# Kernel tuning notes

Measured on AMD Instinct MI355X. Metric: run time of the kernel, lower is better.

Reference implementation:

```python
import jax, jax.numpy as jnp
import numpy as np

B, S, D, H, KD = 4, 2048, 640, 10, 64


def setup_inputs() -> dict:
    key = jax.random.key(0)
    k0, k1, k2, k3, k4 = jax.random.split(key, 5)
    x = jax.random.normal(k0, (B, S, D), dtype=jnp.float32)
    # per-head projection weights, stacked over heads: [H, D, KD]
    Wq = jax.random.normal(k1, (H, D, KD), dtype=jnp.float32) * 0.05
    Wk = jax.random.normal(k2, (H, D, KD), dtype=jnp.float32) * 0.05
    Wv = jax.random.normal(k3, (H, D, KD), dtype=jnp.float32) * 0.05
    # output projection: [H*KD, D]
    Wo = jax.random.normal(k4, (H * KD, D), dtype=jnp.float32) * 0.05
    return {"x": x, "Wq": Wq, "Wk": Wk, "Wv": Wv, "Wo": Wo}


def reference(x, Wq, Wk, Wv, Wo):
    # Batched equivalent of the per-head Python loop:
    # each head computes q=x@Wq_h, k=x@Wk_h, v=x@Wv_h, softmax(q k^T / sqrt(KD)) @ v
    q = jnp.einsum("bsd,hdk->bhsk", x, Wq)
    k = jnp.einsum("bsd,hdk->bhsk", x, Wk)
    v = jnp.einsum("bsd,hdk->bhsk", x, Wv)
    scale = 1.0 / jnp.sqrt(jnp.asarray(KD, x.dtype))
    scores = jnp.einsum("bhsk,bhtk->bhst", q, k) * scale  # [B,H,S,S]
    attn = jax.nn.softmax(scores, axis=-1)
    z = jnp.einsum("bhst,bhtk->bhsk", attn, v)  # [B,H,S,KD]
    # concat heads along last axis (head 0 first, matching the loop order)
    z = z.transpose(0, 2, 1, 3).reshape(x.shape[0], x.shape[1], H * KD)
    return jnp.einsum("bsf,fd->bsd", z, Wo)
```

## Files before the change

kernel.cpp:

```cpp
#include <hip/hip_runtime.h>
#include <hip/hip_bf16.h>

#define B_  4
#define S_  2048
#define D_  640
#define H_  10
#define KD_ 64

typedef __attribute__((ext_vector_type(8))) short  short8;
typedef __attribute__((ext_vector_type(4))) short  short4v;
typedef __attribute__((ext_vector_type(4))) float  floatx4;
typedef __attribute__((ext_vector_type(2))) unsigned int uint2v;
typedef __attribute__((ext_vector_type(4))) unsigned int uint4v;

static __device__ __forceinline__ short f2bf_fast(float f) {
    unsigned int u = __float_as_uint(f);
    u += 0x7fffu + ((u >> 16) & 1u);
    return (short)(u >> 16);
}
static __device__ __forceinline__ unsigned int pack2bf(float a, float b) {
    union { __hip_bfloat162 h; unsigned int u; } c;
    c.h = __float22bfloat162_rn(float2{a, b});
    return c.u;
}
static __device__ __forceinline__ float bf2f(short v) {
    return __uint_as_float(((unsigned int)(unsigned short)v) << 16);
}

static __device__ __forceinline__ void gload_lds16(const void* gp, void* lp) {
    __builtin_amdgcn_global_load_lds(
        (const __attribute__((address_space(1))) unsigned int*)gp,
        (__attribute__((address_space(3))) unsigned int*)lp, 16, 0, 0);
}

__global__ __launch_bounds__(256) void prep(
        const float* __restrict__ x,
        const float* __restrict__ Wq, const float* __restrict__ Wk,
        const float* __restrict__ Wv, const float* __restrict__ Wo,
        short* __restrict__ xb, short* __restrict__ BigT,
        short* __restrict__ WoT) {
    __shared__ float tile[32][33];
    int bid = blockIdx.x;
    if (bid < 5120) {
        int idx = (bid * 256 + threadIdx.x) * 4;
        float4 v = *(const float4*)(x + idx);
        uint2v o;
        o[0] = pack2bf(v.x, v.y);
        o[1] = pack2bf(v.z, v.w);
        *(uint2v*)(xb + idx) = o;
    } else if (bid < 6320) {
        int flat = bid - 5120;
        int bz = flat / 40, rem = flat % 40;
        int by = rem >> 1, bxx = rem & 1;
        int w = bz / 10, h = bz % 10;
        const float* W = ((w == 0) ? Wq : (w == 1) ? Wk : Wv) + h * 640 * 64;
        short* out = BigT + (w * 640 + h * 64) * 640;
        int c0 = bxx * 32;
        int r0 = by * 32;
        int tx = threadIdx.x & 31, ty = threadIdx.x >> 5;
        #pragma unroll
        for (int k = 0; k < 4; ++k)
            tile[ty + 8 * k][tx] = W[(r0 + ty + 8 * k) * 64 + c0 + tx];
        __syncthreads();
        #pragma unroll
        for (int k = 0; k < 4; ++k)
            out[(c0 + ty + 8 * k) * 640 + r0 + tx] = f2bf_fast(tile[tx][ty + 8 * k]);
    } else {
        int flat = bid - 6320;
        int c0 = (flat % 20) * 32;
        int r0 = (flat / 20) * 32;
        int tx = threadIdx.x & 31, ty = threadIdx.x >> 5;
        #pragma unroll
        for (int k = 0; k < 4; ++k)
            tile[ty + 8 * k][tx] = Wo[(r0 + ty + 8 * k) * 640 + c0 + tx];
        __syncthreads();
        #pragma unroll
        for (int k = 0; k < 4; ++k)
            WoT[(c0 + ty + 8 * k) * 640 + r0 + tx] = f2bf_fast(tile[tx][ty + 8 * k]);
    }
}


__global__ __launch_bounds__(256) void qkv_gemm(
        const short* __restrict__ X, const short* __restrict__ BigT,
        short* __restrict__ qb, short* __restrict__ kb, short* __restrict__ vtb) {
    __shared__ __align__(16) short Ab[2][128][32];
    __shared__ __align__(16) short Bb[2][128][32];

    int wave = threadIdx.x >> 6;
    int lane = threadIdx.x & 63;
    int lq = lane & 15, quad = lane >> 4;
    int wm = (wave & 1) * 64, wn = (wave >> 1) * 64;

    int lin = blockIdx.y * 64 + blockIdx.x;
    int tm = ((lin & 7) * 8 + ((lin >> 3) & 7)) * 128;
    int tn = (lin >> 6) * 128;

    int srow = lane >> 2;
    int schunk = (lane & 3) ^ ((lane >> 3) & 3);
    const short* Asrc0 = X    + (tm + wave * 32 + srow) * 640 + schunk * 8;
    const short* Bsrc0 = BigT + (tn + wave * 32 + srow) * 640 + schunk * 8;
    const short* Asrc1 = Asrc0 + 16 * 640;
    const short* Bsrc1 = Bsrc0 + 16 * 640;

    floatx4 acc[4][4];
    for (int a = 0; a < 4; ++a)
        for (int n = 0; n < 4; ++n)
            acc[a][n] = (floatx4){0.f, 0.f, 0.f, 0.f};

    int rsw = (lq >> 1) & 3;

    gload_lds16(Asrc0, &Ab[0][wave * 32][0]);
    gload_lds16(Asrc1, &Ab[0][wave * 32 + 16][0]);
    gload_lds16(Bsrc0, &Bb[0][wave * 32][0]);
    gload_lds16(Bsrc1, &Bb[0][wave * 32 + 16][0]);

    int p = 0;
    bool isV = (tn >= 1280);

    for (int k0 = 0; k0 < 640; k0 += 32) {
        __syncthreads();
        if (k0 + 32 < 640) {
            int pn = p ^ 1;
            gload_lds16(Asrc0 + k0 + 32, &Ab[pn][wave * 32][0]);
            gload_lds16(Asrc1 + k0 + 32, &Ab[pn][wave * 32 + 16][0]);
            gload_lds16(Bsrc0 + k0 + 32, &Bb[pn][wave * 32][0]);
            gload_lds16(Bsrc1 + k0 + 32, &Bb[pn][wave * 32 + 16][0]);
        }

        short8 af[4], bf[4];
        #pragma unroll
        for (int t = 0; t < 4; ++t) {
            af[t] = *(const short8*)(&Ab[p][wm + t * 16 + lq][(quad ^ rsw) * 8]);
            bf[t] = *(const short8*)(&Bb[p][wn + t * 16 + lq][(quad ^ rsw) * 8]);
        }
        if (!isV) {
            #pragma unroll
            for (int mt = 0; mt < 4; ++mt)
                #pragma unroll
                for (int nt = 0; nt < 4; ++nt)
                    acc[mt][nt] = __builtin_amdgcn_mfma_f32_16x16x32_bf16(
                        bf[nt], af[mt], acc[mt][nt], 0, 0, 0);
        } else {
            #pragma unroll
            for (int mt = 0; mt < 4; ++mt)
                #pragma unroll
                for (int nt = 0; nt < 4; ++nt)
                    acc[mt][nt] = __builtin_amdgcn_mfma_f32_16x16x32_bf16(
                        af[mt], bf[nt], acc[mt][nt], 0, 0, 0);
        }
        p ^= 1;
    }

    if (!isV) {
        const float qscale = 0.18033688011112042f;
        short* dst = (tn < 640) ? qb : kb;
        float scale = (tn < 640) ? qscale : 1.0f;
        #pragma unroll
        for (int nt = 0; nt < 4; ++nt) {
            int rem = (tn + wn + nt * 16) % 640;
            int hh = rem / 64;
            int kd0 = (rem % 64) + quad * 4;
            #pragma unroll
            for (int mt = 0; mt < 4; ++mt) {
                int m = tm + wm + mt * 16 + lq;
                int b = m >> 11, s = m & 2047;
                uint2v w;
                w[0] = pack2bf(acc[mt][nt][0] * scale, acc[mt][nt][1] * scale);
                w[1] = pack2bf(acc[mt][nt][2] * scale, acc[mt][nt][3] * scale);
                *(uint2v*)(dst + (((b * H_ + hh) * S_ + s) * KD_ + kd0)) = w;
            }
        }
    } else {
        #pragma unroll
        for (int nt = 0; nt < 4; ++nt) {
            int rem = (tn + wn + nt * 16) - 1280;
            int hh = rem / 64;
            int kd = (rem % 64) + lq;
            #pragma unroll
            for (int mt = 0; mt < 4; ++mt) {
                int s = tm + wm + mt * 16 + quad * 4;
                int b = s >> 11, s0 = s & 2047;
                uint2v w;
                w[0] = pack2bf(acc[mt][nt][0], acc[mt][nt][1]);
                w[1] = pack2bf(acc[mt][nt][2], acc[mt][nt][3]);
                *(uint2v*)(vtb + (((b * H_ + hh) * KD_ + kd) * (long)S_ + s0)) = w;
            }
        }
    }
}

__global__ __launch_bounds__(256, 3) void attn(
        const short* __restrict__ qb, const short* __restrict__ kbuf,
        const short* __restrict__ vtb, short* __restrict__ zp0,
        short* __restrict__ zp1, float* __restrict__ lsvb) {
    __shared__ __align__(16) short Kbuf[2][64][64];
    __shared__ __align__(16) short Vbuf[2][64][64];

    int wave = threadIdx.x >> 6;
    int lane = threadIdx.x & 63;
    int lq = lane & 15, quad = lane >> 4;

    int bx = blockIdx.x;
    int xcd = bx & 7, slot = bx >> 3;
    int bh = xcd * 5 + (slot >> 5);
    int rest = slot & 31;
    int qt = rest >> 1;
    int half = rest & 1;
    int b = bh / 10, h = bh % 10;
    int q0 = qt * 128;

    const short* qp = qb + (b * H_ + h) * S_ * KD_;
    const short* kp = kbuf + (b * H_ + h) * S_ * KD_ + half * 1024 * KD_;
    const short* vp = vtb + (b * H_ + h) * KD_ * S_ + half * 1024;

    int r8 = lane >> 3;
    int g  = (lane & 7) ^ r8;
    const short* kg0 = kp + (wave * 16 + r8) * 64 + g * 8;
    const short* kg1 = kp + (wave * 16 + 8 + r8) * 64 + g * 8;
    const short* vg0 = vp + (wave * 16 + r8) * (long)S_ + g * 8;
    const short* vg1 = vp + (wave * 16 + 8 + r8) * (long)S_ + g * 8;

    short8 qA0, qA1, qB0, qB1;
    {
        int rowA = q0 + wave * 32 + lq;
        qA0 = *(const short8*)(qp + rowA * 64 + quad * 8);
        qA1 = *(const short8*)(qp + rowA * 64 + 32 + quad * 8);
        qB0 = *(const short8*)(qp + (rowA + 16) * 64 + quad * 8);
        qB1 = *(const short8*)(qp + (rowA + 16) * 64 + 32 + quad * 8);
    }

    short8 ones;
    #pragma unroll
    for (int i = 0; i < 8; ++i) ones[i] = (short)0x3F80;

    floatx4 OA[4], OB[4];
    for (int n = 0; n < 4; ++n) {
        OA[n] = (floatx4){0.f, 0.f, 0.f, 0.f};
        OB[n] = (floatx4){0.f, 0.f, 0.f, 0.f};
    }
    floatx4 lsvA = (floatx4){0.f, 0.f, 0.f, 0.f};
    floatx4 lsvB = (floatx4){0.f, 0.f, 0.f, 0.f};

    gload_lds16(kg0, &Kbuf[0][wave * 16][0]);
    gload_lds16(kg1, &Kbuf[0][wave * 16 + 8][0]);
    gload_lds16(vg0, &Vbuf[0][wave * 16][0]);
    gload_lds16(vg1, &Vbuf[0][wave * 16 + 8][0]);

    int p = 0;
    int sw = lq & 7;

    for (int t0 = 0; t0 < 1024; t0 += 64) {
        __syncthreads();

        if (t0 + 64 < 1024) {
            int pn = p ^ 1;
            gload_lds16(kg0 + (t0 + 64) * 64, &Kbuf[pn][wave * 16][0]);
            gload_lds16(kg1 + (t0 + 64) * 64, &Kbuf[pn][wave * 16 + 8][0]);
            gload_lds16(vg0 + (t0 + 64),      &Vbuf[pn][wave * 16][0]);
            gload_lds16(vg1 + (t0 + 64),      &Vbuf[pn][wave * 16 + 8][0]);
        }

        const short* Kb = &Kbuf[p][0][0];
        const short* Vb = &Vbuf[p][0][0];

        floatx4 sTA[4], sTB[4];
        __builtin_amdgcn_s_setprio(1);
        #pragma unroll
        for (int kblk = 0; kblk < 4; ++kblk) {
            const short* krow = Kb + (kblk * 16 + lq) * 64;
            short8 bk0 = *(const short8*)(krow + (quad ^ sw) * 8);
            short8 bk1 = *(const short8*)(krow + ((quad + 4) ^ sw) * 8);
            floatx4 zA = (floatx4){0.f, 0.f, 0.f, 0.f};
            zA = __builtin_amdgcn_mfma_f32_16x16x32_bf16(bk0, qA0, zA, 0, 0, 0);
            sTA[kblk] = __builtin_amdgcn_mfma_f32_16x16x32_bf16(bk1, qA1, zA, 0, 0, 0);
            floatx4 zB = (floatx4){0.f, 0.f, 0.f, 0.f};
            zB = __builtin_amdgcn_mfma_f32_16x16x32_bf16(bk0, qB0, zB, 0, 0, 0);
            sTB[kblk] = __builtin_amdgcn_mfma_f32_16x16x32_bf16(bk1, qB1, zB, 0, 0, 0);
        }
        __builtin_amdgcn_s_setprio(0);

        #pragma unroll
        for (int ts = 0; ts < 2; ++ts) {
            int ka = ts * 2, kc = ts * 2 + 1;
            unsigned int a00 = pack2bf(__builtin_amdgcn_exp2f(sTA[ka][0]),
                                       __builtin_amdgcn_exp2f(sTA[ka][1]));
            unsigned int a01 = pack2bf(__builtin_amdgcn_exp2f(sTA[ka][2]),
                                       __builtin_amdgcn_exp2f(sTA[ka][3]));
            unsigned int a10 = pack2bf(__builtin_amdgcn_exp2f(sTA[kc][0]),
                                       __builtin_amdgcn_exp2f(sTA[kc][1]));
            unsigned int a11 = pack2bf(__builtin_amdgcn_exp2f(sTA[kc][2]),
                                       __builtin_amdgcn_exp2f(sTA[kc][3]));
            uint2v sa0 = __builtin_amdgcn_permlane32_swap(a00, a10, false, false);
            uint2v sa1 = __builtin_amdgcn_permlane32_swap(a01, a11, false, false);
            uint2v wa02 = __builtin_amdgcn_permlane16_swap(sa0[0], sa0[1], false, false);
            uint2v wa13 = __builtin_amdgcn_permlane16_swap(sa1[0], sa1[1], false, false);
            union { unsigned int u[4]; short8 s8; } pfa;
            pfa.u[0] = wa02[0];
            pfa.u[1] = wa13[0];
            pfa.u[2] = wa02[1];
            pfa.u[3] = wa13[1];
            short8 pfA = pfa.s8;
            unsigned int b00 = pack2bf(__builtin_amdgcn_exp2f(sTB[ka][0]),
                                       __builtin_amdgcn_exp2f(sTB[ka][1]));
            unsigned int b01 = pack2bf(__builtin_amdgcn_exp2f(sTB[ka][2]),
                                       __builtin_amdgcn_exp2f(sTB[ka][3]));
            unsigned int b10 = pack2bf(__builtin_amdgcn_exp2f(sTB[kc][0]),
                                       __builtin_amdgcn_exp2f(sTB[kc][1]));
            unsigned int b11 = pack2bf(__builtin_amdgcn_exp2f(sTB[kc][2]),
                                       __builtin_amdgcn_exp2f(sTB[kc][3]));
            uint2v sb0 = __builtin_amdgcn_permlane32_swap(b00, b10, false, false);
            uint2v sb1 = __builtin_amdgcn_permlane32_swap(b01, b11, false, false);
            uint2v wb02 = __builtin_amdgcn_permlane16_swap(sb0[0], sb0[1], false, false);
            uint2v wb13 = __builtin_amdgcn_permlane16_swap(sb1[0], sb1[1], false, false);
            union { unsigned int u[4]; short8 s8; } pfb;
            pfb.u[0] = wb02[0];
            pfb.u[1] = wb13[0];
            pfb.u[2] = wb02[1];
            pfb.u[3] = wb13[1];
            short8 pfB = pfb.s8;

            __builtin_amdgcn_s_setprio(1);
            lsvA = __builtin_amdgcn_mfma_f32_16x16x32_bf16(ones, pfA, lsvA, 0, 0, 0);
            lsvB = __builtin_amdgcn_mfma_f32_16x16x32_bf16(ones, pfB, lsvB, 0, 0, 0);
            #pragma unroll
            for (int db = 0; db < 4; ++db) {
                const short* vrow = Vb + (db * 16 + lq) * 64;
                short8 bv = *(const short8*)(vrow + ((ts * 4 + quad) ^ sw) * 8);
                OA[db] = __builtin_amdgcn_mfma_f32_16x16x32_bf16(bv, pfA, OA[db], 0, 0, 0);
                OB[db] = __builtin_amdgcn_mfma_f32_16x16x32_bf16(bv, pfB, OB[db], 0, 0, 0);
            }
            __builtin_amdgcn_s_setprio(0);
        }

        p ^= 1;
    }

    short* dst = half ? zp1 : zp0;
    int sA = q0 + wave * 32 + lq;
    int sB = sA + 16;
    short* zrA = dst + (b * S_ + sA) * 640 + h * 64;
    short* zrB = dst + (b * S_ + sB) * 640 + h * 64;
    #pragma unroll
    for (int db = 0; db < 4; ++db) {
        uint2v za, zv;
        za[0] = pack2bf(OA[db][0], OA[db][1]);
        za[1] = pack2bf(OA[db][2], OA[db][3]);
        *(uint2v*)(zrA + db * 16 + quad * 4) = za;
        zv[0] = pack2bf(OB[db][0], OB[db][1]);
        zv[1] = pack2bf(OB[db][2], OB[db][3]);
        *(uint2v*)(zrB + db * 16 + quad * 4) = zv;
    }
    if (quad == 0) {
        float* lp = lsvb + half * (B_ * H_ * S_) + (b * H_ + h) * S_;
        lp[sA] = lsvA[0];
        lp[sB] = lsvB[0];
    }
}

__global__ __launch_bounds__(256) void combine(
        const short* __restrict__ zp1, const float* __restrict__ lsvb,
        short* __restrict__ zb) {
    int idx = blockIdx.x * 256 + threadIdx.x;
    int row = idx / 80;
    int col = (idx - row * 80) * 8;
    int b = row >> 11, s = row & 2047;
    int h = col >> 6;
    int li = (b * H_ + h) * S_ + s;
    float inv = 1.0f / (lsvb[li] + lsvb[B_ * H_ * S_ + li]);

    const short* a0 = zb  + row * 640 + col;
    const short* a1 = zp1 + row * 640 + col;
    short8 p0 = *(const short8*)a0;
    short8 p1 = *(const short8*)a1;
    float f[8];
    #pragma unroll
    for (int i = 0; i < 8; ++i)
        f[i] = (bf2f(p0[i]) + bf2f(p1[i])) * inv;
    uint4v o;
    o[0] = pack2bf(f[0], f[1]);
    o[1] = pack2bf(f[2], f[3]);
    o[2] = pack2bf(f[4], f[5]);
    o[3] = pack2bf(f[6], f[7]);
    *(uint4v*)(zb + row * 640 + col) = o;
}

__global__ __launch_bounds__(256) void out_gemm(
        const short* __restrict__ Z, const short* __restrict__ WoT,
        float* __restrict__ out) {
    __shared__ __align__(16) short Ab[2][128][32];
    __shared__ __align__(16) short Bb[2][64][32];

    int wave = threadIdx.x >> 6;
    int lane = threadIdx.x & 63;
    int lq = lane & 15, quad = lane >> 4;
    int wm = (wave & 1) * 64;
    int wn = (wave >> 1) * 32;

    int lin = blockIdx.y * 64 + blockIdx.x;
    int tm = ((lin & 7) * 8 + ((lin >> 3) & 7)) * 128;
    int tn = (lin >> 6) * 64;

    int srow = lane >> 2;
    int schunk = (lane & 3) ^ ((lane >> 3) & 3);
    const short* Asrc0 = Z   + (tm + wave * 32 + srow) * 640 + schunk * 8;
    const short* Asrc1 = Asrc0 + 16 * 640;
    const short* Bsrc0 = WoT + (tn + wave * 16 + srow) * 640 + schunk * 8;

    floatx4 acc[4][2];
    for (int a = 0; a < 4; ++a)
        for (int n = 0; n < 2; ++n)
            acc[a][n] = (floatx4){0.f, 0.f, 0.f, 0.f};

    int rsw = (lq >> 1) & 3;

    gload_lds16(Asrc0, &Ab[0][wave * 32][0]);
    gload_lds16(Asrc1, &Ab[0][wave * 32 + 16][0]);
    gload_lds16(Bsrc0, &Bb[0][wave * 16][0]);

    int p = 0;
    for (int k0 = 0; k0 < 640; k0 += 32) {
        __syncthreads();
        if (k0 + 32 < 640) {
            int pn = p ^ 1;
            gload_lds16(Asrc0 + k0 + 32, &Ab[pn][wave * 32][0]);
            gload_lds16(Asrc1 + k0 + 32, &Ab[pn][wave * 32 + 16][0]);
            gload_lds16(Bsrc0 + k0 + 32, &Bb[pn][wave * 16][0]);
        }

        short8 af[4], bf[2];
        #pragma unroll
        for (int t = 0; t < 4; ++t)
            af[t] = *(const short8*)(&Ab[p][wm + t * 16 + lq][(quad ^ rsw) * 8]);
        #pragma unroll
        for (int u = 0; u < 2; ++u)
            bf[u] = *(const short8*)(&Bb[p][wn + u * 16 + lq][(quad ^ rsw) * 8]);
        #pragma unroll
        for (int mt = 0; mt < 4; ++mt)
            #pragma unroll
            for (int nt = 0; nt < 2; ++nt)
                acc[mt][nt] = __builtin_amdgcn_mfma_f32_16x16x32_bf16(
                    bf[nt], af[mt], acc[mt][nt], 0, 0, 0);
        p ^= 1;
    }

    #pragma unroll
    for (int mt = 0; mt < 4; ++mt) {
        int m = tm + wm + mt * 16 + lq;
        #pragma unroll
        for (int nt = 0; nt < 2; ++nt) {
            int n0 = tn + wn + nt * 16 + quad * 4;
            float4 v;
            v.x = acc[mt][nt][0];
            v.y = acc[mt][nt][1];
            v.z = acc[mt][nt][2];
            v.w = acc[mt][nt][3];
            *(float4*)(out + m * 640 + n0) = v;
        }
    }
}

extern "C" void kernel_launch(void* const* d_in, const int* in_sizes, int n_in,
                              void* d_out, int out_size, void* d_ws, size_t ws_size,
                              hipStream_t stream) {
    const float* x  = (const float*)d_in[0];
    const float* Wq = (const float*)d_in[1];
    const float* Wk = (const float*)d_in[2];
    const float* Wv = (const float*)d_in[3];
    const float* Wo = (const float*)d_in[4];
    float* out = (float*)d_out;

    char* ws = (char*)d_ws;
    short* BigT = (short*)(ws);
    short* WoT  = (short*)(ws + 2457600);
    short* xb   = (short*)(ws + 3276800);
    short* qb   = (short*)(ws + 13762560);
    short* kb   = (short*)(ws + 24248320);
    short* vtb  = (short*)(ws + 34734080);
    short* zb   = (short*)(ws + 45219840);
    short* zp1  = xb;
    float* lsvb = (float*)ws;

    prep<<<dim3(6720), dim3(256), 0, stream>>>(x, Wq, Wk, Wv, Wo, xb, BigT, WoT);
    qkv_gemm<<<dim3(64, 15), dim3(256), 0, stream>>>(xb, BigT, qb, kb, vtb);
    attn<<<dim3(1280), dim3(256), 0, stream>>>(qb, kb, vtb, zb, zp1, lsvb);
    combine<<<dim3(2560), dim3(256), 0, stream>>>(zp1, lsvb, zb);
    out_gemm<<<dim3(64, 10), dim3(256), 0, stream>>>(zb, WoT, out);
}
```

Before: 192.5 us.

## Fuse attention partial combine into output projection GEMM A-tile loads

Result: slower. 197.2 us (+2.4%).

```diff
diff --git a/kernel.cpp b/kernel.cpp
--- a/kernel.cpp
+++ b/kernel.cpp
@@ -358,38 +358,13 @@
     }
 }
 
-__global__ __launch_bounds__(256) void combine(
-        const short* __restrict__ zp1, const float* __restrict__ lsvb,
-        short* __restrict__ zb) {
-    int idx = blockIdx.x * 256 + threadIdx.x;
-    int row = idx / 80;
-    int col = (idx - row * 80) * 8;
-    int b = row >> 11, s = row & 2047;
-    int h = col >> 6;
-    int li = (b * H_ + h) * S_ + s;
-    float inv = 1.0f / (lsvb[li] + lsvb[B_ * H_ * S_ + li]);
-
-    const short* a0 = zb  + row * 640 + col;
-    const short* a1 = zp1 + row * 640 + col;
-    short8 p0 = *(const short8*)a0;
-    short8 p1 = *(const short8*)a1;
-    float f[8];
-    #pragma unroll
-    for (int i = 0; i < 8; ++i)
-        f[i] = (bf2f(p0[i]) + bf2f(p1[i])) * inv;
-    uint4v o;
-    o[0] = pack2bf(f[0], f[1]);
-    o[1] = pack2bf(f[2], f[3]);
-    o[2] = pack2bf(f[4], f[5]);
-    o[3] = pack2bf(f[6], f[7]);
-    *(uint4v*)(zb + row * 640 + col) = o;
-}
-
 __global__ __launch_bounds__(256) void out_gemm(
-        const short* __restrict__ Z, const short* __restrict__ WoT,
+        const short* __restrict__ P0, const short* __restrict__ P1,
+        const float* __restrict__ lsvb, const short* __restrict__ WoT,
         float* __restrict__ out) {
     __shared__ __align__(16) short Ab[2][128][32];
     __shared__ __align__(16) short Bb[2][64][32];
+    __shared__ float invS[128][10];
 
     int wave = threadIdx.x >> 6;
     int lane = threadIdx.x & 63;
@@ -401,10 +376,20 @@
     int tm = ((lin & 7) * 8 + ((lin >> 3) & 7)) * 128;
     int tn = (lin >> 6) * 64;
 
+    for (int i = threadIdx.x; i < 1280; i += 256) {
+        int r = i / 10, hh = i - r * 10;
+        int m = tm + r, bb = m >> 11, ss = m & 2047;
+        int li = (bb * H_ + hh) * S_ + ss;
+        invS[r][hh] = 1.0f / (lsvb[li] + lsvb[B_ * H_ * S_ + li]);
+    }
+
     int srow = lane >> 2;
     int schunk = (lane & 3) ^ ((lane >> 3) & 3);
-    const short* Asrc0 = Z   + (tm + wave * 32 + srow) * 640 + schunk * 8;
-    const short* Asrc1 = Asrc0 + 16 * 640;
+    int lrow0 = wave * 32 + srow;
+    int lrow1 = lrow0 + 16;
+    int dcol = (lane & 3) * 8;
+    const short* A0s = P0 + (tm + lrow0) * 640 + schunk * 8;
+    const short* A1s = P1 + (tm + lrow0) * 640 + schunk * 8;
     const short* Bsrc0 = WoT + (tn + wave * 16 + srow) * 640 + schunk * 8;
 
     floatx4 acc[4][2];
@@ -414,18 +399,43 @@
 
     int rsw = (lq >> 1) & 3;
 
-    gload_lds16(Asrc0, &Ab[0][wave * 32][0]);
-    gload_lds16(Asrc1, &Ab[0][wave * 32 + 16][0]);
-    gload_lds16(Bsrc0, &Bb[0][wave * 16][0]);
+    #define COMBINE8(dst8, xa, ya, s) do { \
+        union { unsigned int u[4]; short8 s8; } cw_; \
+        _Pragma("unroll") \
+        for (int j_ = 0; j_ < 4; ++j_) \
+            cw_.u[j_] = pack2bf((bf2f((xa)[2 * j_]) + bf2f((ya)[2 * j_])) * (s), \
+                                (bf2f((xa)[2 * j_ + 1]) + bf2f((ya)[2 * j_ + 1])) * (s)); \
+        dst8 = cw_.s8; \
+    } while (0)
+
+    __syncthreads();
+
+    {
+        short8 x0 = *(const short8*)(A0s);
+        short8 y0 = *(const short8*)(A1s);
+        short8 x1 = *(const short8*)(A0s + 16 * 640);
+        short8 y1 = *(const short8*)(A1s + 16 * 640);
+        gload_lds16(Bsrc0, &Bb[0][wave * 16][0]);
+        float i0 = invS[lrow0][0], i1 = invS[lrow1][0];
+        short8 w0, w1;
+        COMBINE8(w0, x0, y0, i0);
+        COMBINE8(w1, x1, y1, i1);
+        *(short8*)(&Ab[0][lrow0][dcol]) = w0;
+        *(short8*)(&Ab[0][lrow1][dcol]) = w1;
+    }
 
     int p = 0;
     for (int k0 = 0; k0 < 640; k0 += 32) {
         __syncthreads();
-        if (k0 + 32 < 640) {
-            int pn = p ^ 1;
-            gload_lds16(Asrc0 + k0 + 32, &Ab[pn][wave * 32][0]);
-            gload_lds16(Asrc1 + k0 + 32, &Ab[pn][wave * 32 + 16][0]);
-            gload_lds16(Bsrc0 + k0 + 32, &Bb[pn][wave * 16][0]);
+
+        short8 x0, y0, x1, y1;
+        bool more = (k0 + 32 < 640);
+        if (more) {
+            x0 = *(const short8*)(A0s + k0 + 32);
+            y0 = *(const short8*)(A1s + k0 + 32);
+            x1 = *(const short8*)(A0s + k0 + 32 + 16 * 640);
+            y1 = *(const short8*)(A1s + k0 + 32 + 16 * 640);
+            gload_lds16(Bsrc0 + k0 + 32, &Bb[p ^ 1][wave * 16][0]);
         }
 
         short8 af[4], bf[2];
@@ -441,8 +451,19 @@
             for (int nt = 0; nt < 2; ++nt)
                 acc[mt][nt] = __builtin_amdgcn_mfma_f32_16x16x32_bf16(
                     bf[nt], af[mt], acc[mt][nt], 0, 0, 0);
+
+        if (more) {
+            int hh = (k0 + 32) >> 6;
+            float i0 = invS[lrow0][hh], i1 = invS[lrow1][hh];
+            short8 w0, w1;
+            COMBINE8(w0, x0, y0, i0);
+            COMBINE8(w1, x1, y1, i1);
+            *(short8*)(&Ab[p ^ 1][lrow0][dcol]) = w0;
+            *(short8*)(&Ab[p ^ 1][lrow1][dcol]) = w1;
+        }
         p ^= 1;
     }
+    #undef COMBINE8
 
     #pragma unroll
     for (int mt = 0; mt < 4; ++mt) {
@@ -484,6 +505,5 @@
     prep<<<dim3(6720), dim3(256), 0, stream>>>(x, Wq, Wk, Wv, Wo, xb, BigT, WoT);
     qkv_gemm<<<dim3(64, 15), dim3(256), 0, stream>>>(xb, BigT, qb, kb, vtb);
     attn<<<dim3(1280), dim3(256), 0, stream>>>(qb, kb, vtb, zb, zp1, lsvb);
-    combine<<<dim3(2560), dim3(256), 0, stream>>>(zp1, lsvb, zb);
-    out_gemm<<<dim3(64, 10), dim3(256), 0, stream>>>(zb, WoT, out);
-}
+    out_gemm<<<dim3(64, 10), dim3(256), 0, stream>>>(zb, zp1, lsvb, WoT, out);
+}
```

## Fuse split-KV combine into output GEMM and transpose MFMA operand order

Applied to the files above, without the earlier changes.

After: 195.3 us. Within noise of the previous version (+1.5%).

```diff
diff --git a/kernel.cpp b/kernel.cpp
--- a/kernel.cpp
+++ b/kernel.cpp
@@ -11,7 +11,6 @@
 typedef __attribute__((ext_vector_type(4))) short  short4v;
 typedef __attribute__((ext_vector_type(4))) float  floatx4;
 typedef __attribute__((ext_vector_type(2))) unsigned int uint2v;
-typedef __attribute__((ext_vector_type(4))) unsigned int uint4v;
 
 static __device__ __forceinline__ short f2bf_fast(float f) {
     unsigned int u = __float_as_uint(f);
@@ -22,9 +21,6 @@
     union { __hip_bfloat162 h; unsigned int u; } c;
     c.h = __float22bfloat162_rn(float2{a, b});
     return c.u;
-}
-static __device__ __forceinline__ float bf2f(short v) {
-    return __uint_as_float(((unsigned int)(unsigned short)v) << 16);
 }
 
 static __device__ __forceinline__ void gload_lds16(const void* gp, void* lp) {
@@ -140,14 +136,14 @@
                 #pragma unroll
                 for (int nt = 0; nt < 4; ++nt)
                     acc[mt][nt] = __builtin_amdgcn_mfma_f32_16x16x32_bf16(
-                        bf[nt], af[mt], acc[mt][nt], 0, 0, 0);
+                        af[mt], bf[nt], acc[mt][nt], 0, 0, 0);
         } else {
             #pragma unroll
-            for (int mt = 0; mt < 4; ++mt)
+            for (int nt = 0; nt < 4; ++nt)
                 #pragma unroll
-                for (int nt = 0; nt < 4; ++nt)
-                    acc[mt][nt] = __builtin_amdgcn_mfma_f32_16x16x32_bf16(
-                        af[mt], bf[nt], acc[mt][nt], 0, 0, 0);
+                for (int mt = 0; mt < 4; ++mt)
+                    acc[nt][mt] = __builtin_amdgcn_mfma_f32_16x16x32_bf16(
+                        bf[nt], af[mt], acc[nt][mt], 0, 0, 0);
         }
         p ^= 1;
     }
@@ -159,32 +155,33 @@
         #pragma unroll
         for (int nt = 0; nt < 4; ++nt) {
             int rem = (tn + wn + nt * 16) % 640;
+            int hh = rem / 64, kd = (rem % 64) + lq;
+            #pragma unroll
+            for (int mt = 0; mt < 4; ++mt) {
+                #pragma unroll
+                for (int r = 0; r < 4; ++r) {
+                    int m = tm + wm + mt * 16 + quad * 4 + r;
+                    int b = m >> 11, s = m & 2047;
+                    dst[((b * H_ + hh) * S_ + s) * KD_ + kd] =
+                        f2bf_fast(acc[mt][nt][r] * scale);
+                }
+            }
+        }
+    } else {
+        #pragma unroll
+        for (int nt = 0; nt < 4; ++nt) {
+            int rem = (tn + wn + nt * 16) - 1280;
             int hh = rem / 64;
             int kd0 = (rem % 64) + quad * 4;
             #pragma unroll
             for (int mt = 0; mt < 4; ++mt) {
                 int m = tm + wm + mt * 16 + lq;
                 int b = m >> 11, s = m & 2047;
-                uint2v w;
-                w[0] = pack2bf(acc[mt][nt][0] * scale, acc[mt][nt][1] * scale);
-                w[1] = pack2bf(acc[mt][nt][2] * scale, acc[mt][nt][3] * scale);
-                *(uint2v*)(dst + (((b * H_ + hh) * S_ + s) * KD_ + kd0)) = w;
-            }
-        }
-    } else {
-        #pragma unroll
-        for (int nt = 0; nt < 4; ++nt) {
-            int rem = (tn + wn + nt * 16) - 1280;
-            int hh = rem / 64;
-            int kd = (rem % 64) + lq;
-            #pragma unroll
-            for (int mt = 0; mt < 4; ++mt) {
-                int s = tm + wm + mt * 16 + quad * 4;
-                int b = s >> 11, s0 = s & 2047;
-                uint2v w;
-                w[0] = pack2bf(acc[mt][nt][0], acc[mt][nt][1]);
-                w[1] = pack2bf(acc[mt][nt][2], acc[mt][nt][3]);
-                *(uint2v*)(vtb + (((b * H_ + hh) * KD_ + kd) * (long)S_ + s0)) = w;
+                #pragma unroll
+                for (int r = 0; r < 4; ++r) {
+                    vtb[((b * H_ + hh) * KD_ + kd0 + r) * S_ + s] =
+                        f2bf_fast(acc[nt][mt][r]);
+                }
             }
         }
     }
@@ -358,38 +355,14 @@
     }
 }
 
-__global__ __launch_bounds__(256) void combine(
-        const short* __restrict__ zp1, const float* __restrict__ lsvb,
-        short* __restrict__ zb) {
-    int idx = blockIdx.x * 256 + threadIdx.x;
-    int row = idx / 80;
-    int col = (idx - row * 80) * 8;
-    int b = row >> 11, s = row & 2047;
-    int h = col >> 6;
-    int li = (b * H_ + h) * S_ + s;
-    float inv = 1.0f / (lsvb[li] + lsvb[B_ * H_ * S_ + li]);
-
-    const short* a0 = zb  + row * 640 + col;
-    const short* a1 = zp1 + row * 640 + col;
-    short8 p0 = *(const short8*)a0;
-    short8 p1 = *(const short8*)a1;
-    float f[8];
-    #pragma unroll
-    for (int i = 0; i < 8; ++i)
-        f[i] = (bf2f(p0[i]) + bf2f(p1[i])) * inv;
-    uint4v o;
-    o[0] = pack2bf(f[0], f[1]);
-    o[1] = pack2bf(f[2], f[3]);
-    o[2] = pack2bf(f[4], f[5]);
-    o[3] = pack2bf(f[6], f[7]);
-    *(uint4v*)(zb + row * 640 + col) = o;
-}
-
 __global__ __launch_bounds__(256) void out_gemm(
-        const short* __restrict__ Z, const short* __restrict__ WoT,
+        const short* __restrict__ P0, const short* __restrict__ P1,
+        const float* __restrict__ lsvb, const short* __restrict__ WoT,
         float* __restrict__ out) {
-    __shared__ __align__(16) short Ab[2][128][32];
+    __shared__ __align__(16) short A0b[2][128][32];
+    __shared__ __align__(16) short A1b[2][128][32];
     __shared__ __align__(16) short Bb[2][64][32];
+    __shared__ float invS[10][128];
 
     int wave = threadIdx.x >> 6;
     int lane = threadIdx.x & 63;
@@ -401,61 +374,93 @@
     int tm = ((lin & 7) * 8 + ((lin >> 3) & 7)) * 128;
     int tn = (lin >> 6) * 64;
 
+    for (int i = threadIdx.x; i < 1280; i += 256) {
+        int hh = i >> 7, r = i & 127;
+        int m = tm + r, bb = m >> 11, ss = m & 2047;
+        int li = (bb * H_ + hh) * S_ + ss;
+        invS[hh][r] = 1.0f / (lsvb[li] + lsvb[B_ * H_ * S_ + li]);
+    }
+
     int srow = lane >> 2;
     int schunk = (lane & 3) ^ ((lane >> 3) & 3);
-    const short* Asrc0 = Z   + (tm + wave * 32 + srow) * 640 + schunk * 8;
-    const short* Asrc1 = Asrc0 + 16 * 640;
+    long aoff = (long)(tm + wave * 32 + srow) * 640 + schunk * 8;
+    const short* A0s = P0 + aoff;
+    const short* A1s = P1 + aoff;
     const short* Bsrc0 = WoT + (tn + wave * 16 + srow) * 640 + schunk * 8;
 
-    floatx4 acc[4][2];
+    floatx4 accS[4][2], accF[4][2];
     for (int a = 0; a < 4; ++a)
-        for (int n = 0; n < 2; ++n)
-            acc[a][n] = (floatx4){0.f, 0.f, 0.f, 0.f};
+        for (int n = 0; n < 2; ++n) {
+            accS[a][n] = (floatx4){0.f, 0.f, 0.f, 0.f};
+            accF[a][n] = (floatx4){0.f, 0.f, 0.f, 0.f};
+        }
 
     int rsw = (lq >> 1) & 3;
 
-    gload_lds16(Asrc0, &Ab[0][wave * 32][0]);
-    gload_lds16(Asrc1, &Ab[0][wave * 32 + 16][0]);
-    gload_lds16(Bsrc0, &Bb[0][wave * 16][0]);
+    gload_lds16(A0s,            &A0b[0][wave * 32][0]);
+    gload_lds16(A0s + 16 * 640, &A0b[0][wave * 32 + 16][0]);
+    gload_lds16(A1s,            &A1b[0][wave * 32][0]);
+    gload_lds16(A1s + 16 * 640, &A1b[0][wave * 32 + 16][0]);
+    gload_lds16(Bsrc0,          &Bb[0][wave * 16][0]);
 
     int p = 0;
     for (int k0 = 0; k0 < 640; k0 += 32) {
         __syncthreads();
         if (k0 + 32 < 640) {
             int pn = p ^ 1;
-            gload_lds16(Asrc0 + k0 + 32, &Ab[pn][wave * 32][0]);
-            gload_lds16(Asrc1 + k0 + 32, &Ab[pn][wave * 32 + 16][0]);
-            gload_lds16(Bsrc0 + k0 + 32, &Bb[pn][wave * 16][0]);
-        }
-
-        short8 af[4], bf[2];
-        #pragma unroll
-        for (int t = 0; t < 4; ++t)
-            af[t] = *(const short8*)(&Ab[p][wm + t * 16 + lq][(quad ^ rsw) * 8]);
+            gload_lds16(A0s + k0 + 32,            &A0b[pn][wave * 32][0]);
+            gload_lds16(A0s + k0 + 32 + 16 * 640, &A0b[pn][wave * 32 + 16][0]);
+            gload_lds16(A1s + k0 + 32,            &A1b[pn][wave * 32][0]);
+            gload_lds16(A1s + k0 + 32 + 16 * 640, &A1b[pn][wave * 32 + 16][0]);
+            gload_lds16(Bsrc0 + k0 + 32,          &Bb[pn][wave * 16][0]);
+        }
+
+        short8 af0[4], af1[4], bf[2];
+        #pragma unroll
+        for (int t = 0; t < 4; ++t) {
+            af0[t] = *(const short8*)(&A0b[p][wm + t * 16 + lq][(quad ^ rsw) * 8]);
+            af1[t] = *(const short8*)(&A1b[p][wm + t * 16 + lq][(quad ^ rsw) * 8]);
+        }
         #pragma unroll
         for (int u = 0; u < 2; ++u)
             bf[u] = *(const short8*)(&Bb[p][wn + u * 16 + lq][(quad ^ rsw) * 8]);
         #pragma unroll
         for (int mt = 0; mt < 4; ++mt)
             #pragma unroll
-            for (int nt = 0; nt < 2; ++nt)
-                acc[mt][nt] = __builtin_amdgcn_mfma_f32_16x16x32_bf16(
-                    bf[nt], af[mt], acc[mt][nt], 0, 0, 0);
+            for (int nt = 0; nt < 2; ++nt) {
+                accS[mt][nt] = __builtin_amdgcn_mfma_f32_16x16x32_bf16(
+                    af0[mt], bf[nt], accS[mt][nt], 0, 0, 0);
+                accS[mt][nt] = __builtin_amdgcn_mfma_f32_16x16x32_bf16(
+                    af1[mt], bf[nt], accS[mt][nt], 0, 0, 0);
+            }
+
+        if (((k0 + 32) & 63) == 0) {
+            int hh = k0 >> 6;
+            #pragma unroll
+            for (int mt = 0; mt < 4; ++mt) {
+                float4 iv = *(const float4*)(&invS[hh][wm + mt * 16 + quad * 4]);
+                #pragma unroll
+                for (int nt = 0; nt < 2; ++nt) {
+                    accF[mt][nt][0] += iv.x * accS[mt][nt][0];
+                    accF[mt][nt][1] += iv.y * accS[mt][nt][1];
+                    accF[mt][nt][2] += iv.z * accS[mt][nt][2];
+                    accF[mt][nt][3] += iv.w * accS[mt][nt][3];
+                    accS[mt][nt] = (floatx4){0.f, 0.f, 0.f, 0.f};
+                }
+            }
+        }
         p ^= 1;
     }
 
     #pragma unroll
     for (int mt = 0; mt < 4; ++mt) {
-        int m = tm + wm + mt * 16 + lq;
         #pragma unroll
         for (int nt = 0; nt < 2; ++nt) {
-            int n0 = tn + wn + nt * 16 + quad * 4;
-            float4 v;
-            v.x = acc[mt][nt][0];
-            v.y = acc[mt][nt][1];
-            v.z = acc[mt][nt][2];
-            v.w = acc[mt][nt][3];
-            *(float4*)(out + m * 640 + n0) = v;
+            #pragma unroll
+            for (int r = 0; r < 4; ++r) {
+                int m = tm + wm + mt * 16 + quad * 4 + r;
+                out[m * 640 + tn + wn + nt * 16 + lq] = accF[mt][nt][r];
+            }
         }
     }
 }
@@ -484,6 +489,5 @@
     prep<<<dim3(6720), dim3(256), 0, stream>>>(x, Wq, Wk, Wv, Wo, xb, BigT, WoT);
     qkv_gemm<<<dim3(64, 15), dim3(256), 0, stream>>>(xb, BigT, qb, kb, vtb);
     attn<<<dim3(1280), dim3(256), 0, stream>>>(qb, kb, vtb, zb, zp1, lsvb);
-    combine<<<dim3(2560), dim3(256), 0, stream>>>(zp1, lsvb, zb);
-    out_gemm<<<dim3(64, 10), dim3(256), 0, stream>>>(zb, WoT, out);
-}
+    out_gemm<<<dim3(64, 10), dim3(256), 0, stream>>>(zb, zp1, lsvb, WoT, out);
+}
```
